# Kernel optimization log

Measured on AMD Instinct MI355X. Metric: run time of the kernel, lower is better.

The kernel has to match this reference:

```python
import jax, jax.numpy as jnp
import numpy as np

B, T, C, H = 4, 2048, 768, 12
D = C // H

def setup_inputs() -> dict:
    key = jax.random.key(0)
    ks = jax.random.split(key, 8)
    s = 1.0 / np.sqrt(C)
    return {
        "x":  jax.random.normal(ks[0], (B, T, C), dtype=jnp.float32),
        "Wq": jax.random.normal(ks[1], (C, C), dtype=jnp.float32) * s,
        "bq": jax.random.normal(ks[2], (C,), dtype=jnp.float32) * 0.02,
        "Wk": jax.random.normal(ks[3], (C, C), dtype=jnp.float32) * s,
        "bk": jax.random.normal(ks[4], (C,), dtype=jnp.float32) * 0.02,
        "Wv": jax.random.normal(ks[5], (C, C), dtype=jnp.float32) * s,
        "bv": jax.random.normal(ks[6], (C,), dtype=jnp.float32) * 0.02,
        "Wp": jax.random.normal(ks[7], (C, C), dtype=jnp.float32) * s,
    }

def reference(x, Wq, bq, Wk, bk, Wv, bv, Wp):
    # Linear projections (torch Linear: y = x @ W.T + b)
    q = x @ Wq.T + bq
    k = x @ Wk.T + bk
    v = x @ Wv.T + bv
    # [B,T,C] -> [B,H,T,D]
    q = q.reshape(B, T, H, D).transpose(0, 2, 1, 3)
    k = k.reshape(B, T, H, D).transpose(0, 2, 1, 3)
    v = v.reshape(B, T, H, D).transpose(0, 2, 1, 3)
    scale = 1.0 / np.sqrt(D).astype(np.float32)
    scores = jnp.einsum('bhqd,bhkd->bhqk', q, k) * scale  # [B,H,T,T]
    attn = jax.nn.softmax(scores, axis=-1)  # no mask in original module
    out = jnp.einsum('bhqk,bhkd->bhqd', attn, v)
    out = out.transpose(0, 2, 1, 3).reshape(B, T, C)
    return out @ Wp.T  # proj has bias=False
```

## Files before the change

kernel.cpp:

```cpp
#include <hip/hip_runtime.h>
#include <hip/hip_bf16.h>
#include <cmath>

constexpr int B  = 4;
constexpr int T  = 2048;
constexpr int C  = 768;
constexpr int H  = 12;
constexpr int Dh = 64;
constexpr int M  = B * T;
constexpr int NQKV = 3 * C;
constexpr int WS2  = C * C;

typedef short bf16x8 __attribute__((ext_vector_type(8)));
typedef short bf16x4 __attribute__((ext_vector_type(4)));
typedef float f32x4  __attribute__((ext_vector_type(4)));
typedef float f32x16 __attribute__((ext_vector_type(16)));

constexpr float SOFT_SCALE = 0.18033688011112042f;

__device__ inline short f2bf(float f) {
    unsigned u = __float_as_uint(f);
    u += 0x7fffu + ((u >> 16) & 1u);
    return (short)(u >> 16);
}

__device__ inline unsigned pk_bf16(float a, float b) {
    __hip_bfloat162 h = __float22bfloat162_rn(float2{a, b});
    return *(unsigned*)&h;
}

__device__ inline bf16x8 mk8(unsigned a, unsigned b, unsigned c, unsigned d) {
    union { unsigned u[4]; bf16x8 v; } x;
    x.u[0] = a; x.u[1] = b; x.u[2] = c; x.u[3] = d;
    return x.v;
}

typedef const __attribute__((address_space(1))) unsigned GU;
typedef __attribute__((address_space(3))) unsigned LU;
__device__ inline void async_copy16(const void* g, void* l) {
    __builtin_amdgcn_global_load_lds((GU*)g, (LU*)l, 16, 0, 0);
}

constexpr size_t XE = (size_t)M * C;
constexpr size_t CV_TOTAL = XE + 4 * (size_t)WS2;

__global__ __launch_bounds__(256)
void convert_all(const float* __restrict__ x,  const float* __restrict__ Wq,
                 const float* __restrict__ Wk, const float* __restrict__ Wv,
                 const float* __restrict__ Wp,
                 short* __restrict__ xb, short* __restrict__ Wqkv,
                 short* __restrict__ Wpb) {
    size_t i = ((size_t)blockIdx.x * 256 + threadIdx.x) * 4;
    const float* src; short* dst; size_t off;
    if (i < XE)                        { src = x;  dst = xb;            off = i; }
    else if (i < XE + WS2)             { src = Wq; dst = Wqkv;          off = i - XE; }
    else if (i < XE + 2 * (size_t)WS2) { src = Wk; dst = Wqkv + WS2;    off = i - XE - WS2; }
    else if (i < XE + 3 * (size_t)WS2) { src = Wv; dst = Wqkv + 2 * WS2; off = i - XE - 2 * (size_t)WS2; }
    else                               { src = Wp; dst = Wpb;           off = i - XE - 3 * (size_t)WS2; }
    float4 v = *(const float4*)(src + off);
    bf16x4 o; o[0] = f2bf(v.x); o[1] = f2bf(v.y); o[2] = f2bf(v.z); o[3] = f2bf(v.w);
    *(bf16x4*)(dst + off) = o;
}

constexpr int BM = 128;

template<int BN_, int WMW, int WNW, int OUT_BF16, int QSCALE>
__global__ __launch_bounds__(256)
void gemm_bt(const short* __restrict__ A, const short* __restrict__ W,
             const float* __restrict__ bias0, const float* __restrict__ bias1,
             const float* __restrict__ bias2,
             void* __restrict__ Yv, int Ndim, int Kdim) {
    constexpr int MT  = BM / WMW / 16;
    constexpr int NT  = BN_ / WNW / 16;
    constexpr int NCH = (BM + BN_) / 16;

    __shared__ short As[2][BM * 32];
    __shared__ short Bs[2][BN_ * 32];

    const int tid  = threadIdx.x;
    const int wave = tid >> 6;
    const int lane = tid & 63;
    const int li   = lane & 15;
    const int quad = lane >> 4;
    const int wm   = wave % WMW;
    const int wn   = wave / WMW;
    const int m0   = blockIdx.y * BM;
    const int n0   = blockIdx.x * BN_;

    f32x4 acc[MT][NT];
    #pragma unroll
    for (int i = 0; i < MT; ++i)
        #pragma unroll
        for (int j = 0; j < NT; ++j)
            acc[i][j] = (f32x4){0.f, 0.f, 0.f, 0.f};

    const int lrow = lane >> 2;
    const int lkof = (lane & 3) * 8;

    for (int k0 = 0; k0 < Kdim; k0 += 64) {
        __syncthreads();
        #pragma unroll
        for (int h = 0; h < 2; ++h)
            #pragma unroll
            for (int ii = 0; ii < NCH / 4; ++ii) {
                int c = ii * 4 + wave;
                if (c < BM / 16)
                    async_copy16(A + (size_t)(m0 + c * 16 + lrow) * Kdim
                                   + k0 + h * 32 + lkof,
                                 &As[h][c * 512]);
                else
                    async_copy16(W + (size_t)(n0 + (c - BM / 16) * 16 + lrow) * Kdim
                                   + k0 + h * 32 + lkof,
                                 &Bs[h][(c - BM / 16) * 512]);
            }
        __syncthreads();

        #pragma unroll
        for (int h = 0; h < 2; ++h) {
            bf16x8 af[MT], bfr[NT];
            #pragma unroll
            for (int t = 0; t < MT; ++t)
                af[t] = *(const bf16x8*)&As[h][(wm * MT * 16 + t * 16 + li) * 32 + quad * 8];
            #pragma unroll
            for (int t = 0; t < NT; ++t)
                bfr[t] = *(const bf16x8*)&Bs[h][(wn * NT * 16 + t * 16 + li) * 32 + quad * 8];
            #pragma unroll
            for (int i = 0; i < MT; ++i)
                #pragma unroll
                for (int j = 0; j < NT; ++j)
                    acc[i][j] = __builtin_amdgcn_mfma_f32_16x16x32_bf16(
                        af[i], bfr[j], acc[i][j], 0, 0, 0);
        }
    }

    float bb[NT];
    #pragma unroll
    for (int nt = 0; nt < NT; ++nt) bb[nt] = 0.f;
    if (bias0) {
        int s = n0 / C;
        const float* bp = (s == 0) ? bias0 : ((s == 1) ? bias1 : bias2);
        int nb = n0 % C;
        #pragma unroll
        for (int nt = 0; nt < NT; ++nt)
            bb[nt] = bp[nb + wn * NT * 16 + nt * 16 + li];
    }

    #pragma unroll
    for (int mt = 0; mt < MT; ++mt)
        #pragma unroll
        for (int nt = 0; nt < NT; ++nt)
            #pragma unroll
            for (int r = 0; r < 4; ++r) {
                int row = m0 + wm * MT * 16 + mt * 16 + quad * 4 + r;
                int col = n0 + wn * NT * 16 + nt * 16 + li;
                float v = acc[mt][nt][r] + bb[nt];
                if constexpr (QSCALE) {
                    if (n0 < C) v *= SOFT_SCALE;
                }
                if constexpr (OUT_BF16)
                    ((short*)Yv)[(size_t)row * Ndim + col] = f2bf(v);
                else
                    ((float*)Yv)[(size_t)row * Ndim + col] = v;
            }
}

constexpr int QT   = 128;
constexpr int KTT  = 64;
constexpr int LSTR = 72;
constexpr int QS   = NQKV;

__global__ __launch_bounds__(256, 3)
void attn_fwd(const short* __restrict__ QKV, short* __restrict__ O) {
    __shared__ short Ks[KTT * LSTR];
    __shared__ short Vt[Dh * LSTR];

    const int tid  = threadIdx.x;
    const int wave = tid >> 6;
    const int lane = tid & 63;
    const int r31  = lane & 31;
    const int hi   = lane >> 5;
    const int b    = blockIdx.z;
    const int h    = blockIdx.y;
    const int qw   = blockIdx.x * QT + wave * 32;

    const short* Qg = QKV + (size_t)(b * T) * QS + h * Dh;
    const short* Kg = QKV + (size_t)(b * T) * QS + C + h * Dh;
    const short* Vg = QKV + (size_t)(b * T) * QS + 2 * C + h * Dh;

    bf16x8 qf[4];
    #pragma unroll
    for (int f = 0; f < 4; ++f)
        qf[f] = *(const bf16x8*)(Qg + (size_t)(qw + r31) * QS + f * 16 + hi * 8);

    bf16x8 ones;
    #pragma unroll
    for (int i = 0; i < 8; ++i) ones[i] = (short)0x3F80;

    f32x16 oacc0 = (f32x16)(0.f);
    f32x16 oacc1 = (f32x16)(0.f);
    f32x16 lacc  = (f32x16)(0.f);

    const int ktok = tid >> 3;
    const int kch  = tid & 7;
    const int vd2  = (tid & 31) * 2;
    const int vg   = tid >> 5;

    int4 kpre[2];
    unsigned vpre[8];
    kpre[0] = *(const int4*)(Kg + (size_t)(ktok)      * QS + kch * 8);
    kpre[1] = *(const int4*)(Kg + (size_t)(ktok + 32) * QS + kch * 8);
    #pragma unroll
    for (int t2 = 0; t2 < 8; ++t2)
        vpre[t2] = *(const unsigned*)(Vg + (size_t)(vg * 8 + t2) * QS + vd2);

    for (int kt = 0; kt < T; kt += KTT) {
        __syncthreads();

        *(int4*)&Ks[ktok * LSTR + kch * 8]        = kpre[0];
        *(int4*)&Ks[(ktok + 32) * LSTR + kch * 8] = kpre[1];
        {
            unsigned lo[4], hh[4];
            #pragma unroll
            for (int j = 0; j < 4; ++j) {
                lo[j] = __builtin_amdgcn_perm(vpre[2 * j + 1], vpre[2 * j], 0x05040100u);
                hh[j] = __builtin_amdgcn_perm(vpre[2 * j + 1], vpre[2 * j], 0x07060302u);
            }
            *(int4*)&Vt[vd2 * LSTR + vg * 8]       = make_int4(lo[0], lo[1], lo[2], lo[3]);
            *(int4*)&Vt[(vd2 + 1) * LSTR + vg * 8] = make_int4(hh[0], hh[1], hh[2], hh[3]);
        }
        __syncthreads();

        if (kt + KTT < T) {
            const size_t nb = kt + KTT;
            kpre[0] = *(const int4*)(Kg + (nb + ktok)      * QS + kch * 8);
            kpre[1] = *(const int4*)(Kg + (nb + ktok + 32) * QS + kch * 8);
            #pragma unroll
            for (int t2 = 0; t2 < 8; ++t2)
                vpre[t2] = *(const unsigned*)(Vg + (nb + vg * 8 + t2) * QS + vd2);
        }

        f32x16 st0 = (f32x16)(0.f);
        f32x16 st1 = (f32x16)(0.f);
        __builtin_amdgcn_s_setprio(1);
        #pragma unroll
        for (int f = 0; f < 4; ++f) {
            bf16x8 k0 = *(const bf16x8*)&Ks[(r31)      * LSTR + f * 16 + hi * 8];
            bf16x8 k1 = *(const bf16x8*)&Ks[(32 + r31) * LSTR + f * 16 + hi * 8];
            st0 = __builtin_amdgcn_mfma_f32_32x32x16_bf16(k0, qf[f], st0, 0, 0, 0);
            st1 = __builtin_amdgcn_mfma_f32_32x32x16_bf16(k1, qf[f], st1, 0, 0, 0);
        }
        __builtin_amdgcn_s_setprio(0);

        #pragma unroll
        for (int kb = 0; kb < 2; ++kb) {
            f32x16 s = kb ? st1 : st0;
            unsigned d[8];
            #pragma unroll
            for (int j = 0; j < 8; ++j) {
                float pa = __builtin_amdgcn_exp2f(s[2 * j]);
                float pb = __builtin_amdgcn_exp2f(s[2 * j + 1]);
                d[j] = pk_bf16(pa, pb);
            }
            auto s02 = __builtin_amdgcn_permlane32_swap(d[0], d[2], false, false);
            auto s13 = __builtin_amdgcn_permlane32_swap(d[1], d[3], false, false);
            auto s46 = __builtin_amdgcn_permlane32_swap(d[4], d[6], false, false);
            auto s57 = __builtin_amdgcn_permlane32_swap(d[5], d[7], false, false);
            bf16x8 pf0 = mk8(s02[0], s13[0], s02[1], s13[1]);
            bf16x8 pf1 = mk8(s46[0], s57[0], s46[1], s57[1]);

            __builtin_amdgcn_s_setprio(1);
            lacc = __builtin_amdgcn_mfma_f32_32x32x16_bf16(pf0, ones, lacc, 0, 0, 0);
            lacc = __builtin_amdgcn_mfma_f32_32x32x16_bf16(pf1, ones, lacc, 0, 0, 0);

            bf16x8 v00 = *(const bf16x8*)&Vt[(r31)      * LSTR + kb * 32 + hi * 8];
            bf16x8 v01 = *(const bf16x8*)&Vt[(r31)      * LSTR + kb * 32 + 16 + hi * 8];
            bf16x8 v10 = *(const bf16x8*)&Vt[(32 + r31) * LSTR + kb * 32 + hi * 8];
            bf16x8 v11 = *(const bf16x8*)&Vt[(32 + r31) * LSTR + kb * 32 + 16 + hi * 8];
            oacc0 = __builtin_amdgcn_mfma_f32_32x32x16_bf16(pf0, v00, oacc0, 0, 0, 0);
            oacc0 = __builtin_amdgcn_mfma_f32_32x32x16_bf16(pf1, v01, oacc0, 0, 0, 0);
            oacc1 = __builtin_amdgcn_mfma_f32_32x32x16_bf16(pf0, v10, oacc1, 0, 0, 0);
            oacc1 = __builtin_amdgcn_mfma_f32_32x32x16_bf16(pf1, v11, oacc1, 0, 0, 0);
            __builtin_amdgcn_s_setprio(0);
        }
    }

    #pragma unroll
    for (int r = 0; r < 16; ++r) {
        float inv = 1.0f / lacc[r];
        int row = (r & 3) + 8 * (r >> 2) + 4 * hi;
        short* op = O + (size_t)(b * T + qw + row) * C + h * Dh + r31;
        op[0]  = f2bf(oacc0[r] * inv);
        op[32] = f2bf(oacc1[r] * inv);
    }
}

extern "C" void kernel_launch(void* const* d_in, const int* in_sizes, int n_in,
                              void* d_out, int out_size, void* d_ws, size_t ws_size,
                              hipStream_t stream) {
    (void)in_sizes; (void)n_in; (void)out_size; (void)ws_size;

    const float* x  = (const float*)d_in[0];
    const float* Wq = (const float*)d_in[1];
    const float* bq = (const float*)d_in[2];
    const float* Wk = (const float*)d_in[3];
    const float* bk = (const float*)d_in[4];
    const float* Wv = (const float*)d_in[5];
    const float* bv = (const float*)d_in[6];
    const float* Wp = (const float*)d_in[7];
    float* out = (float*)d_out;

    short* xb    = (short*)d_ws;
    short* Wqkv  = xb + (size_t)M * C;
    short* Wpb   = Wqkv + 3 * (size_t)WS2;
    short* QKVb  = Wpb + (size_t)WS2;
    short* AOb   = QKVb + (size_t)M * NQKV;

    convert_all<<<dim3(CV_TOTAL / 1024), 256, 0, stream>>>(
        x, Wq, Wk, Wv, Wp, xb, Wqkv, Wpb);

    gemm_bt<128, 2, 2, 1, 1><<<dim3(NQKV / 128, M / BM), 256, 0, stream>>>(
        xb, Wqkv, bq, bk, bv, QKVb, NQKV, C);

    attn_fwd<<<dim3(T / QT, H, B), 256, 0, stream>>>(QKVb, AOb);

    gemm_bt<64, 4, 1, 0, 0><<<dim3(C / 64, M / BM), 256, 0, stream>>>(
        AOb, Wpb, nullptr, nullptr, nullptr, out, C, C);
}
```

Before: 236.3 us.

## Split attention key range across two wave groups with shared-memory reduction

Each attention block now runs 512 threads: two groups of four waves cover the same 128 query rows, and each group processes half of the key/value sequence through its own K/V staging buffers. At the end, the second group writes its partial output and row-sum accumulators to shared memory and the first group adds them before normalising and storing. The aim is more waves per block for latency hiding and twice the concurrent K/V streaming per block. It costs more shared memory, an extra reduction pass with two barriers, and the 512-thread, 6-waves launch bound tightens the per-thread register budget.

```diff
diff --git a/kernel.cpp b/kernel.cpp
--- a/kernel.cpp
+++ b/kernel.cpp
@@ -168,20 +168,29 @@
 constexpr int KTT  = 64;
 constexpr int LSTR = 72;
 constexpr int QS   = NQKV;
-
-__global__ __launch_bounds__(256, 3)
+constexpr int KHT  = T / 2;
+
+__global__ __launch_bounds__(512, 6)
 void attn_fwd(const short* __restrict__ QKV, short* __restrict__ O) {
-    __shared__ short Ks[KTT * LSTR];
-    __shared__ short Vt[Dh * LSTR];
+    __shared__ short smem[25088];
 
     const int tid  = threadIdx.x;
     const int wave = tid >> 6;
     const int lane = tid & 63;
     const int r31  = lane & 31;
     const int hi   = lane >> 5;
+    const int qs   = wave & 3;
+    const int kh   = wave >> 2;
+    const int strm = tid >> 8;
+    const int t8   = tid & 255;
     const int b    = blockIdx.z;
     const int h    = blockIdx.y;
-    const int qw   = blockIdx.x * QT + wave * 32;
+    const int qrow = blockIdx.x * QT + qs * 32;
+
+    short* KsS = smem + strm * 4608;
+    short* VtS = smem + 9216 + strm * 4608;
+    const short* KsC = smem + kh * 4608;
+    const short* VtC = smem + 9216 + kh * 4608;
 
     const short* Qg = QKV + (size_t)(b * T) * QS + h * Dh;
     const short* Kg = QKV + (size_t)(b * T) * QS + C + h * Dh;
@@ -190,7 +199,7 @@
     bf16x8 qf[4];
     #pragma unroll
     for (int f = 0; f < 4; ++f)
-        qf[f] = *(const bf16x8*)(Qg + (size_t)(qw + r31) * QS + f * 16 + hi * 8);
+        qf[f] = *(const bf16x8*)(Qg + (size_t)(qrow + r31) * QS + f * 16 + hi * 8);
 
     bf16x8 ones;
     #pragma unroll
@@ -200,24 +209,25 @@
     f32x16 oacc1 = (f32x16)(0.f);
     f32x16 lacc  = (f32x16)(0.f);
 
-    const int ktok = tid >> 3;
-    const int kch  = tid & 7;
-    const int vd2  = (tid & 31) * 2;
-    const int vg   = tid >> 5;
+    const int ktok = t8 >> 3;
+    const int kch  = t8 & 7;
+    const int vd2  = (t8 & 31) * 2;
+    const int vg   = t8 >> 5;
+    const int tbS  = strm * KHT;
 
     int4 kpre[2];
     unsigned vpre[8];
-    kpre[0] = *(const int4*)(Kg + (size_t)(ktok)      * QS + kch * 8);
-    kpre[1] = *(const int4*)(Kg + (size_t)(ktok + 32) * QS + kch * 8);
+    kpre[0] = *(const int4*)(Kg + (size_t)(tbS + ktok)      * QS + kch * 8);
+    kpre[1] = *(const int4*)(Kg + (size_t)(tbS + ktok + 32) * QS + kch * 8);
     #pragma unroll
     for (int t2 = 0; t2 < 8; ++t2)
-        vpre[t2] = *(const unsigned*)(Vg + (size_t)(vg * 8 + t2) * QS + vd2);
-
-    for (int kt = 0; kt < T; kt += KTT) {
+        vpre[t2] = *(const unsigned*)(Vg + (size_t)(tbS + vg * 8 + t2) * QS + vd2);
+
+    for (int ktl = 0; ktl < KHT; ktl += KTT) {
         __syncthreads();
 
-        *(int4*)&Ks[ktok * LSTR + kch * 8]        = kpre[0];
-        *(int4*)&Ks[(ktok + 32) * LSTR + kch * 8] = kpre[1];
+        *(int4*)&KsS[ktok * LSTR + kch * 8]        = kpre[0];
+        *(int4*)&KsS[(ktok + 32) * LSTR + kch * 8] = kpre[1];
         {
             unsigned lo[4], hh[4];
             #pragma unroll
@@ -225,13 +235,13 @@
                 lo[j] = __builtin_amdgcn_perm(vpre[2 * j + 1], vpre[2 * j], 0x05040100u);
                 hh[j] = __builtin_amdgcn_perm(vpre[2 * j + 1], vpre[2 * j], 0x07060302u);
             }
-            *(int4*)&Vt[vd2 * LSTR + vg * 8]       = make_int4(lo[0], lo[1], lo[2], lo[3]);
-            *(int4*)&Vt[(vd2 + 1) * LSTR + vg * 8] = make_int4(hh[0], hh[1], hh[2], hh[3]);
+            *(int4*)&VtS[vd2 * LSTR + vg * 8]       = make_int4(lo[0], lo[1], lo[2], lo[3]);
+            *(int4*)&VtS[(vd2 + 1) * LSTR + vg * 8] = make_int4(hh[0], hh[1], hh[2], hh[3]);
         }
         __syncthreads();
 
-        if (kt + KTT < T) {
-            const size_t nb = kt + KTT;
+        if (ktl + KTT < KHT) {
+            const size_t nb = tbS + ktl + KTT;
             kpre[0] = *(const int4*)(Kg + (nb + ktok)      * QS + kch * 8);
             kpre[1] = *(const int4*)(Kg + (nb + ktok + 32) * QS + kch * 8);
             #pragma unroll
@@ -244,8 +254,8 @@
         __builtin_amdgcn_s_setprio(1);
         #pragma unroll
         for (int f = 0; f < 4; ++f) {
-            bf16x8 k0 = *(const bf16x8*)&Ks[(r31)      * LSTR + f * 16 + hi * 8];
-            bf16x8 k1 = *(const bf16x8*)&Ks[(32 + r31) * LSTR + f * 16 + hi * 8];
+            bf16x8 k0 = *(const bf16x8*)&KsC[(r31)      * LSTR + f * 16 + hi * 8];
+            bf16x8 k1 = *(const bf16x8*)&KsC[(32 + r31) * LSTR + f * 16 + hi * 8];
             st0 = __builtin_amdgcn_mfma_f32_32x32x16_bf16(k0, qf[f], st0, 0, 0, 0);
             st1 = __builtin_amdgcn_mfma_f32_32x32x16_bf16(k1, qf[f], st1, 0, 0, 0);
         }
@@ -272,10 +282,10 @@
             lacc = __builtin_amdgcn_mfma_f32_32x32x16_bf16(pf0, ones, lacc, 0, 0, 0);
             lacc = __builtin_amdgcn_mfma_f32_32x32x16_bf16(pf1, ones, lacc, 0, 0, 0);
 
-            bf16x8 v00 = *(const bf16x8*)&Vt[(r31)      * LSTR + kb * 32 + hi * 8];
-            bf16x8 v01 = *(const bf16x8*)&Vt[(r31)      * LSTR + kb * 32 + 16 + hi * 8];
-            bf16x8 v10 = *(const bf16x8*)&Vt[(32 + r31) * LSTR + kb * 32 + hi * 8];
-            bf16x8 v11 = *(const bf16x8*)&Vt[(32 + r31) * LSTR + kb * 32 + 16 + hi * 8];
+            bf16x8 v00 = *(const bf16x8*)&VtC[(r31)      * LSTR + kb * 32 + hi * 8];
+            bf16x8 v01 = *(const bf16x8*)&VtC[(r31)      * LSTR + kb * 32 + 16 + hi * 8];
+            bf16x8 v10 = *(const bf16x8*)&VtC[(32 + r31) * LSTR + kb * 32 + hi * 8];
+            bf16x8 v11 = *(const bf16x8*)&VtC[(32 + r31) * LSTR + kb * 32 + 16 + hi * 8];
             oacc0 = __builtin_amdgcn_mfma_f32_32x32x16_bf16(pf0, v00, oacc0, 0, 0, 0);
             oacc0 = __builtin_amdgcn_mfma_f32_32x32x16_bf16(pf1, v01, oacc0, 0, 0, 0);
             oacc1 = __builtin_amdgcn_mfma_f32_32x32x16_bf16(pf0, v10, oacc1, 0, 0, 0);
@@ -284,13 +294,31 @@
         }
     }
 
-    #pragma unroll
-    for (int r = 0; r < 16; ++r) {
-        float inv = 1.0f / lacc[r];
-        int row = (r & 3) + 8 * (r >> 2) + 4 * hi;
-        short* op = O + (size_t)(b * T + qw + row) * C + h * Dh + r31;
-        op[0]  = f2bf(oacc0[r] * inv);
-        op[32] = f2bf(oacc1[r] * inv);
+    __syncthreads();
+    float* red = (float*)smem;
+    if (kh == 1) {
+        int base = ((wave - 4) * 64 + lane) * 49;
+        #pragma unroll
+        for (int r = 0; r < 16; ++r) {
+            red[base + r]      = oacc0[r];
+            red[base + 16 + r] = oacc1[r];
+            red[base + 32 + r] = lacc[r];
+        }
+    }
+    __syncthreads();
+    if (kh == 0) {
+        int base = (wave * 64 + lane) * 49;
+        #pragma unroll
+        for (int r = 0; r < 16; ++r) {
+            float o0 = oacc0[r] + red[base + r];
+            float o1 = oacc1[r] + red[base + 16 + r];
+            float l  = lacc[r]  + red[base + 32 + r];
+            float inv = 1.0f / l;
+            int row = (r & 3) + 8 * (r >> 2) + 4 * hi;
+            short* op = O + (size_t)(b * T + qrow + row) * C + h * Dh + r31;
+            op[0]  = f2bf(o0 * inv);
+            op[32] = f2bf(o1 * inv);
+        }
     }
 }
 
@@ -321,7 +349,7 @@
     gemm_bt<128, 2, 2, 1, 1><<<dim3(NQKV / 128, M / BM), 256, 0, stream>>>(
         xb, Wqkv, bq, bk, bv, QKVb, NQKV, C);
 
-    attn_fwd<<<dim3(T / QT, H, B), 256, 0, stream>>>(QKVb, AOb);
+    attn_fwd<<<dim3(T / QT, H, B), 512, 0, stream>>>(QKVb, AOb);
 
     gemm_bt<64, 4, 1, 0, 0><<<dim3(C / 64, M / BM), 256, 0, stream>>>(
         AOb, Wpb, nullptr, nullptr, nullptr, out, C, C);
```

After: 751.0 us. 218% more time.
